# Kernel optimization log

Hardware: AMD Instinct MI355X
Metric: run time of the kernel (lower is better)

## Reference

```python
import jax, jax.numpy as jnp
import numpy as np

DIM = 768
N_HEADS = 12
HEAD_DIM = DIM // N_HEADS
SCALE = HEAD_DIM ** (-0.5)


def setup_inputs() -> dict:
    key = jax.random.key(0)
    k1, k2, k3 = jax.random.split(key, 3)
    B, S = 8, 1024
    x = jax.random.normal(k1, (B, S, DIM), dtype=jnp.float32)
    qkv_w = jax.random.normal(k2, (3 * DIM, DIM), dtype=jnp.float32) * (DIM ** -0.5)
    qkv_b = jnp.zeros((3 * DIM,), dtype=jnp.float32)
    proj_w = jax.random.normal(k3, (DIM, DIM), dtype=jnp.float32) * (DIM ** -0.5)
    proj_b = jnp.zeros((DIM,), dtype=jnp.float32)
    return {"x": x, "qkv_w": qkv_w, "qkv_b": qkv_b, "proj_w": proj_w, "proj_b": proj_b}


def reference(x, qkv_w, qkv_b, proj_w, proj_b):
    B, S, D = x.shape
    # qkv projection: (B,S,3D)
    qkv = jnp.einsum('bsd,ed->bse', x, qkv_w) + qkv_b
    qkv = qkv.reshape(B, S, 3, N_HEADS, HEAD_DIM)
    q, k, v = qkv[:, :, 0], qkv[:, :, 1], qkv[:, :, 2]  # each (B,S,H,Dh)
    # scaled dot-product attention, materializing (B,H,S,S) as the original does
    scores = jnp.einsum('bqhd,bkhd->bhqk', q, k) * SCALE
    attn = jax.nn.softmax(scores, axis=-1)
    out = jnp.einsum('bhqk,bkhd->bqhd', attn, v).reshape(B, S, D)
    # output projection
    return jnp.einsum('bsd,ed->bse', out, proj_w) + proj_b
```

## Files before the change

### kernel.cpp

```cpp
#include <hip/hip_runtime.h>
#include <hip/hip_bf16.h>


typedef __attribute__((ext_vector_type(4))) float  f32x4;
typedef __attribute__((ext_vector_type(8))) short  short8;
typedef __attribute__((ext_vector_type(4))) short  short4v;

__device__ __forceinline__ unsigned short f2bf_hw(float f) {
  return __builtin_bit_cast(unsigned short, __float2bfloat16(f));
}

#define MFMA16(a, b, c) __builtin_amdgcn_mfma_f32_16x16x32_bf16((a), (b), (c), 0, 0, 0)

#define QSCALE 0.18033688011112042f

__device__ __forceinline__ void gload_lds16(const unsigned short* g, char* lds) {
  __builtin_amdgcn_global_load_lds(
      (const __attribute__((address_space(1))) unsigned int*)g,
      (__attribute__((address_space(3))) unsigned int*)lds, 16, 0, 0);
}

__global__ __launch_bounds__(256)
void cvt3(const float* __restrict__ a, unsigned short* __restrict__ da, int na,
          const float* __restrict__ b, unsigned short* __restrict__ db, int nb,
          const float* __restrict__ c, unsigned short* __restrict__ dc)
{
  int i = blockIdx.x * 256 + threadIdx.x;
  const float* s; unsigned short* d;
  if (i < na)           { s = a; d = da; }
  else if (i < na + nb) { s = b; d = db; i -= na; }
  else                  { s = c; d = dc; i -= na + nb; }
  f32x4 v = ((const f32x4*)s)[i];
  short4v h;
  h[0] = (short)f2bf_hw(v[0]); h[1] = (short)f2bf_hw(v[1]);
  h[2] = (short)f2bf_hw(v[2]); h[3] = (short)f2bf_hw(v[3]);
  ((short4v*)d)[i] = h;
}

template<int EPI>
__global__ __launch_bounds__(256)
void gemm_bt(const unsigned short* __restrict__ A, const unsigned short* __restrict__ Wb,
             const float* __restrict__ bias,
             unsigned short* __restrict__ Qt, unsigned short* __restrict__ Kt,
             unsigned short* __restrict__ Vt, float* __restrict__ Out)
{
  __shared__ char lds[65536];
  const int tid = threadIdx.x;
  const int w = tid >> 6, l = tid & 63, lr = l & 15, lg = l >> 4;
  const int wr = w >> 1, wc = w & 1;
  const int m0 = blockIdx.x * 128, n0 = blockIdx.y * 128;
  f32x4 acc[4][4] = {};

  const int srow = tid >> 3;
  const int cb   = ((tid & 7) << 4) ^ ((srow & 7) << 4);
  const unsigned short* pA = A  + (size_t)(m0 + srow) * 768 + (cb >> 1);
  const unsigned short* pW = Wb + (size_t)(n0 + srow) * 768 + (cb >> 1);
  char* const ldsA = lds + tid * 16;
  char* const ldsW = lds + 16384 + tid * 16;

  #pragma unroll
  for (int c = 0; c < 4; ++c) gload_lds16(pA + c * 32 * 768, ldsA + c * 4096);
  #pragma unroll
  for (int c = 0; c < 4; ++c) gload_lds16(pW + c * 32 * 768, ldsW + c * 4096);
  pA += 64; pW += 64;

  for (int kt = 0; kt < 12; ++kt) {
    if (kt < 11) {
      const int nb = ((kt + 1) & 1) * 32768;
      #pragma unroll
      for (int c = 0; c < 4; ++c) gload_lds16(pA + c * 32 * 768, ldsA + nb + c * 4096);
      #pragma unroll
      for (int c = 0; c < 4; ++c) gload_lds16(pW + c * 32 * 768, ldsW + nb + c * 4096);
      pA += 64; pW += 64;
      asm volatile("s_waitcnt vmcnt(8)" ::: "memory");
    } else {
      asm volatile("s_waitcnt vmcnt(0)" ::: "memory");
    }
    __builtin_amdgcn_s_barrier();
    __builtin_amdgcn_sched_barrier(0);

    const char* Ab = lds + (kt & 1) * 32768;
    const char* Bb = Ab + 16384;
    #pragma unroll
    for (int kc = 0; kc < 2; ++kc) {
      short8 af[4], bfr[4];
      #pragma unroll
      for (int mf = 0; mf < 4; ++mf) {
        const int row = wr * 64 + mf * 16 + lr;
        af[mf] = *(const short8*)(Ab + row * 128 +
                                  ((kc * 64 + lg * 16) ^ ((row & 7) << 4)));
      }
      #pragma unroll
      for (int nf = 0; nf < 4; ++nf) {
        const int row = wc * 64 + nf * 16 + lr;
        bfr[nf] = *(const short8*)(Bb + row * 128 +
                                   ((kc * 64 + lg * 16) ^ ((row & 7) << 4)));
      }
      #pragma unroll
      for (int mf = 0; mf < 4; ++mf)
        #pragma unroll
        for (int nf = 0; nf < 4; ++nf)
          acc[mf][nf] = MFMA16(af[mf], bfr[nf], acc[mf][nf]);
    }
    __builtin_amdgcn_s_barrier();
  }

  if constexpr (EPI == 0) {
    const int tt = blockIdx.y / 6;
    const int h = (blockIdx.y % 6) * 2 + wc;
    #pragma unroll
    for (int nf = 0; nf < 4; ++nf) {
      const int dh = nf * 16 + lr;
      const float bv = bias[n0 + wc * 64 + dh];
      #pragma unroll
      for (int mf = 0; mf < 4; ++mf) {
        const int mb = m0 + wr * 64 + mf * 16 + lg * 4;
        const int b_ = mb >> 10, s_ = mb & 1023;
        f32x4 c = acc[mf][nf];
        if (tt == 0) {
          unsigned short* p = Qt + ((b_ * 12 + h) * 1024 + s_) * 64 + dh;
          #pragma unroll
          for (int j = 0; j < 4; ++j) p[j * 64] = f2bf_hw((c[j] + bv) * QSCALE);
        } else if (tt == 1) {
          unsigned short* p = Kt + ((b_ * 12 + h) * 1024 + s_) * 64 + dh;
          #pragma unroll
          for (int j = 0; j < 4; ++j) p[j * 64] = f2bf_hw(c[j] + bv);
        } else {
          short4v pk;
          #pragma unroll
          for (int j = 0; j < 4; ++j) pk[j] = (short)f2bf_hw(c[j] + bv);
          *(short4v*)(Vt + ((b_ * 12 + h) * 64 + dh) * 1024 + s_) = pk;
        }
      }
    }
  } else {
    #pragma unroll
    for (int nf = 0; nf < 4; ++nf) {
      const int e = n0 + wc * 64 + nf * 16 + lr;
      const float bv = bias[e];
      #pragma unroll
      for (int mf = 0; mf < 4; ++mf) {
        const int mb = m0 + wr * 64 + mf * 16 + lg * 4;
        #pragma unroll
        for (int j = 0; j < 4; ++j)
          Out[(size_t)(mb + j) * 768 + e] = acc[mf][nf][j] + bv;
      }
    }
  }
}

__global__ __launch_bounds__(256, 2)
void attn_fwd(const unsigned short* __restrict__ Qt,
              const unsigned short* __restrict__ Kt,
              const unsigned short* __restrict__ Vt,
              unsigned short* __restrict__ AO)
{
  __shared__ char lds[81920];
  char* Ks = lds;
  char* Vs = lds + 32768;
  char* Ps = lds + 65536;

  const int bid = blockIdx.x;
  const int bh = bid % 96, qt = bid / 96;
  const int tid = threadIdx.x, w = tid >> 6, l = tid & 63, lr = l & 15, lg = l >> 4;
  const int q0 = qt * 64 + w * 16;
  const unsigned short* Qh = Qt + bh * 65536;
  const unsigned short* Kh = Kt + bh * 65536;
  const unsigned short* Vh = Vt + bh * 65536;

  const int krow0 = tid >> 3, kcb0 = (tid & 7) << 4;
  const int vrow0 = tid >> 4, vcb0 = (tid & 15) << 4;

  const short8 aq0 = *(const short8*)(Qh + (q0 + lr) * 64 + lg * 8);
  const short8 aq1 = *(const short8*)(Qh + (q0 + lr) * 64 + 32 + lg * 8);

  #pragma unroll
  for (int c = 0; c < 4; ++c) {
    const int row = krow0 + c * 32;
    const int cb = kcb0 ^ ((row & 7) << 4);
    gload_lds16(Kh + (size_t)row * 64 + (cb >> 1), Ks + tid * 16 + c * 4096);
  }
  #pragma unroll
  for (int c = 0; c < 4; ++c) {
    const int row = vrow0 + c * 16;
    const int cb = vcb0 ^ ((row & 7) << 4);
    gload_lds16(Vh + (size_t)row * 1024 + (cb >> 1), Vs + tid * 16 + c * 4096);
  }
  __syncthreads();

  float mr = -1e30f, lsum = 0.f;
  f32x4 o[4] = {};
  char* Pw = Ps + w * 4096;

  for (int t = 0; t < 8; ++t) {
    const int cur = t & 1;
    if (t < 7) {
      const int ktn = (t + 1) * 128;
      #pragma unroll
      for (int c = 0; c < 4; ++c) {
        const int row = krow0 + c * 32;
        const int cb = kcb0 ^ ((row & 7) << 4);
        gload_lds16(Kh + (size_t)(ktn + row) * 64 + (cb >> 1),
                    Ks + (cur ^ 1) * 16384 + tid * 16 + c * 4096);
      }
      #pragma unroll
      for (int c = 0; c < 4; ++c) {
        const int row = vrow0 + c * 16;
        const int cb = vcb0 ^ ((row & 7) << 4);
        gload_lds16(Vh + (size_t)row * 1024 + ktn + (cb >> 1),
                    Vs + (cur ^ 1) * 16384 + tid * 16 + c * 4096);
      }
    }

    const char* Kb = Ks + cur * 16384;
    f32x4 sf[8];
    __builtin_amdgcn_s_setprio(1);
    #pragma unroll
    for (int kf = 0; kf < 8; ++kf) {
      const int row = kf * 16 + lr;
      const char* base = Kb + row * 128;
      const int swz = (row & 7) << 4;
      short8 b0 = *(const short8*)(base + ((lg * 16) ^ swz));
      short8 b1 = *(const short8*)(base + ((64 + lg * 16) ^ swz));
      f32x4 c = {};
      c = MFMA16(b0, aq0, c);
      c = MFMA16(b1, aq1, c);
      sf[kf] = c;
    }
    __builtin_amdgcn_s_setprio(0);

    float tm = sf[0][0];
    #pragma unroll
    for (int kf = 0; kf < 8; ++kf)
      #pragma unroll
      for (int j = 0; j < 4; ++j) tm = fmaxf(tm, sf[kf][j]);
    tm = fmaxf(tm, __shfl_xor(tm, 16));
    tm = fmaxf(tm, __shfl_xor(tm, 32));

    const float mn = fmaxf(mr, tm);
    const float corr = exp2f(mr - mn);
    float ts = 0.f;
    const int pswz = (lr & 7) << 4;
    #pragma unroll
    for (int kf = 0; kf < 8; ++kf) {
      short4v pk;
      #pragma unroll
      for (int j = 0; j < 4; ++j) {
        float p = exp2f(sf[kf][j] - mn);
        ts += p;
        pk[j] = (short)f2bf_hw(p);
      }
      *(short4v*)(Pw + lr * 256 + ((kf * 32 + lg * 8) ^ pswz)) = pk;
    }
    ts += __shfl_xor(ts, 16);
    ts += __shfl_xor(ts, 32);
    lsum = lsum * corr + ts;
    mr = mn;

    float cj[4];
    #pragma unroll
    for (int j = 0; j < 4; ++j) cj[j] = __shfl(corr, lg * 4 + j);
    #pragma unroll
    for (int cf = 0; cf < 4; ++cf)
      #pragma unroll
      for (int j = 0; j < 4; ++j) o[cf][j] *= cj[j];

    asm volatile("s_waitcnt lgkmcnt(0)" ::: "memory");
    __builtin_amdgcn_sched_barrier(0);

    const char* Vb = Vs + cur * 16384;
    __builtin_amdgcn_s_setprio(1);
    #pragma unroll
    for (int kc = 0; kc < 4; ++kc) {
      short8 pa = *(const short8*)(Pw + lr * 256 + ((kc * 64 + lg * 16) ^ pswz));
      #pragma unroll
      for (int cf = 0; cf < 4; ++cf) {
        const int row = cf * 16 + lr;
        short8 bv = *(const short8*)(Vb + row * 256 +
                                     ((kc * 64 + lg * 16) ^ ((row & 7) << 4)));
        o[cf] = MFMA16(pa, bv, o[cf]);
      }
    }
    __builtin_amdgcn_s_setprio(0);

    __syncthreads();
  }

  const float inv = 1.f / lsum;
  float ij[4];
  #pragma unroll
  for (int j = 0; j < 4; ++j) ij[j] = __shfl(inv, lg * 4 + j);
  const int b_ = bh / 12, h = bh % 12;
  #pragma unroll
  for (int cf = 0; cf < 4; ++cf)
    #pragma unroll
    for (int j = 0; j < 4; ++j)
      AO[(b_ * 1024 + q0 + lg * 4 + j) * 768 + h * 64 + cf * 16 + lr] = f2bf_hw(o[cf][j] * ij[j]);
}

extern "C" void kernel_launch(void* const* d_in, const int* in_sizes, int n_in,
                              void* d_out, int out_size, void* d_ws, size_t ws_size,
                              hipStream_t stream)
{
  const float* x      = (const float*)d_in[0];
  const float* qkv_w  = (const float*)d_in[1];
  const float* qkv_b  = (const float*)d_in[2];
  const float* proj_w = (const float*)d_in[3];
  const float* proj_b = (const float*)d_in[4];
  float* out = (float*)d_out;

  unsigned short* ws = (unsigned short*)d_ws;
  unsigned short* xb  = ws;
  unsigned short* Qt  = ws + 6291456;
  unsigned short* Kt  = Qt + 6291456;
  unsigned short* Vt  = Kt + 6291456;
  unsigned short* qwb = Vt + 6291456;
  unsigned short* pwb = qwb + 1769472;
  unsigned short* AO  = xb;

  cvt3<<<8448, 256, 0, stream>>>(x, xb, 1572864, qkv_w, qwb, 442368, proj_w, pwb);
  gemm_bt<0><<<dim3(64, 18), 256, 0, stream>>>(xb, qwb, qkv_b, Qt, Kt, Vt, nullptr);
  attn_fwd<<<1536, 256, 0, stream>>>(Qt, Kt, Vt, AO);
  gemm_bt<1><<<dim3(64, 6), 256, 0, stream>>>(AO, pwb, proj_b, nullptr, nullptr, nullptr, out);
}
```

Measured before the change: 126.6 us.

## Restructure attention: smaller KV tiles, two query sub-tiles per block, lazy rescale

The attention kernel now streams K/V in 64-key tiles instead of 128, which halves LDS use and raises the occupancy hint from 2 to 4 blocks per CU. Each block handles two 64-row query sub-tiles in sequence, and the K/V pipeline wraps around so the first tile of the second pass is prefetched. The grid is halved to match. Online-softmax rescaling is skipped unless the running max grows by more than 8 (in log2 units), the PV MFMA operands are swapped so output writes are packed per row, and the P tile is packed as bf16 pairs. The cost is twice as many loop iterations and barriers per key length, plus fewer blocks to spread across CUs.

```diff
diff --git a/kernel.cpp b/kernel.cpp
--- a/kernel.cpp
+++ b/kernel.cpp
@@ -5,9 +5,13 @@
 typedef __attribute__((ext_vector_type(4))) float  f32x4;
 typedef __attribute__((ext_vector_type(8))) short  short8;
 typedef __attribute__((ext_vector_type(4))) short  short4v;
+typedef __attribute__((ext_vector_type(2))) unsigned int uint2v;
 
 __device__ __forceinline__ unsigned short f2bf_hw(float f) {
   return __builtin_bit_cast(unsigned short, __float2bfloat16(f));
+}
+__device__ __forceinline__ unsigned int pk2bf(float a, float b) {
+  return (unsigned int)f2bf_hw(a) | ((unsigned int)f2bf_hw(b) << 16);
 }
 
 #define MFMA16(a, b, c) __builtin_amdgcn_mfma_f32_16x16x32_bf16((a), (b), (c), 0, 0, 0)
@@ -149,153 +153,141 @@
   }
 }
 
-__global__ __launch_bounds__(256, 2)
+__global__ __launch_bounds__(256, 4)
 void attn_fwd(const unsigned short* __restrict__ Qt,
               const unsigned short* __restrict__ Kt,
               const unsigned short* __restrict__ Vt,
               unsigned short* __restrict__ AO)
 {
-  __shared__ char lds[81920];
+  __shared__ char lds[40960];
   char* Ks = lds;
-  char* Vs = lds + 32768;
-  char* Ps = lds + 65536;
+  char* Vs = lds + 16384;
+  char* Ps = lds + 32768;
 
   const int bid = blockIdx.x;
   const int bh = bid % 96, qt = bid / 96;
   const int tid = threadIdx.x, w = tid >> 6, l = tid & 63, lr = l & 15, lg = l >> 4;
-  const int q0 = qt * 64 + w * 16;
   const unsigned short* Qh = Qt + bh * 65536;
   const unsigned short* Kh = Kt + bh * 65536;
   const unsigned short* Vh = Vt + bh * 65536;
-
-  const int krow0 = tid >> 3, kcb0 = (tid & 7) << 4;
-  const int vrow0 = tid >> 4, vcb0 = (tid & 15) << 4;
-
-  const short8 aq0 = *(const short8*)(Qh + (q0 + lr) * 64 + lg * 8);
-  const short8 aq1 = *(const short8*)(Qh + (q0 + lr) * 64 + 32 + lg * 8);
+  const int b_ = bh / 12, h = bh % 12;
+
+  const int srow = tid >> 3;
+  const int cb   = ((tid & 7) << 4) ^ ((srow & 7) << 4);
+  char* const ldsK = Ks + tid * 16;
+  char* const ldsV = Vs + tid * 16;
+  char* const Pw = Ps + w * 2048;
+  const int pswz = (lr & 7) << 4;
 
   #pragma unroll
-  for (int c = 0; c < 4; ++c) {
-    const int row = krow0 + c * 32;
-    const int cb = kcb0 ^ ((row & 7) << 4);
-    gload_lds16(Kh + (size_t)row * 64 + (cb >> 1), Ks + tid * 16 + c * 4096);
+  for (int c = 0; c < 2; ++c)
+    gload_lds16(Kh + (size_t)(srow + c * 32) * 64 + (cb >> 1), ldsK + c * 4096);
+  #pragma unroll
+  for (int c = 0; c < 2; ++c)
+    gload_lds16(Vh + (size_t)(srow + c * 32) * 1024 + (cb >> 1), ldsV + c * 4096);
+  __syncthreads();
+
+  for (int qs = 0; qs < 2; ++qs) {
+    const int q0 = qt * 128 + qs * 64 + w * 16;
+    const short8 aq0 = *(const short8*)(Qh + (q0 + lr) * 64 + lg * 8);
+    const short8 aq1 = *(const short8*)(Qh + (q0 + lr) * 64 + 32 + lg * 8);
+
+    float mr = -1e30f, lsum = 0.f;
+    f32x4 o[4] = {};
+
+    for (int t = 0; t < 16; ++t) {
+      const int cur = t & 1;
+      if (!(qs == 1 && t == 15)) {
+        const int nk = ((t + 1) & 15) * 64;
+        const int nb = (cur ^ 1) * 8192;
+        #pragma unroll
+        for (int c = 0; c < 2; ++c)
+          gload_lds16(Kh + (size_t)(nk + srow + c * 32) * 64 + (cb >> 1),
+                      ldsK + nb + c * 4096);
+        #pragma unroll
+        for (int c = 0; c < 2; ++c)
+          gload_lds16(Vh + (size_t)(srow + c * 32) * 1024 + nk + (cb >> 1),
+                      ldsV + nb + c * 4096);
+      }
+
+      const char* Kb = Ks + cur * 8192;
+      f32x4 sf[4];
+      __builtin_amdgcn_s_setprio(1);
+      #pragma unroll
+      for (int kf = 0; kf < 4; ++kf) {
+        const char* base = Kb + (kf * 16 + lr) * 128;
+        short8 b0 = *(const short8*)(base + ((lg * 16) ^ pswz));
+        short8 b1 = *(const short8*)(base + ((64 + lg * 16) ^ pswz));
+        f32x4 c = {};
+        c = MFMA16(b0, aq0, c);
+        c = MFMA16(b1, aq1, c);
+        sf[kf] = c;
+      }
+      __builtin_amdgcn_s_setprio(0);
+
+      float tm = fmaxf(fmaxf(sf[0][0], sf[0][1]), fmaxf(sf[0][2], sf[0][3]));
+      #pragma unroll
+      for (int kf = 1; kf < 4; ++kf)
+        tm = fmaxf(tm, fmaxf(fmaxf(sf[kf][0], sf[kf][1]), fmaxf(sf[kf][2], sf[kf][3])));
+      tm = fmaxf(tm, __shfl_xor(tm, 16));
+      tm = fmaxf(tm, __shfl_xor(tm, 32));
+
+      if (__any(tm > mr + 8.0f)) {
+        const float mn = fmaxf(mr, tm);
+        const float corr = exp2f(mr - mn);
+        lsum *= corr;
+        #pragma unroll
+        for (int cf = 0; cf < 4; ++cf)
+          #pragma unroll
+          for (int j = 0; j < 4; ++j) o[cf][j] *= corr;
+        mr = mn;
+      }
+
+      float ts = 0.f;
+      #pragma unroll
+      for (int kf = 0; kf < 4; ++kf) {
+        const float p0 = exp2f(sf[kf][0] - mr);
+        const float p1 = exp2f(sf[kf][1] - mr);
+        const float p2 = exp2f(sf[kf][2] - mr);
+        const float p3 = exp2f(sf[kf][3] - mr);
+        ts += (p0 + p1) + (p2 + p3);
+        uint2v pv; pv[0] = pk2bf(p0, p1); pv[1] = pk2bf(p2, p3);
+        *(uint2v*)(Pw + lr * 128 + ((kf * 32 + lg * 8) ^ pswz)) = pv;
+      }
+      ts += __shfl_xor(ts, 16);
+      ts += __shfl_xor(ts, 32);
+      lsum += ts;
+
+      asm volatile("s_waitcnt lgkmcnt(0)" ::: "memory");
+      __builtin_amdgcn_sched_barrier(0);
+
+      const char* Vb = Vs + cur * 8192;
+      __builtin_amdgcn_s_setprio(1);
+      #pragma unroll
+      for (int kc = 0; kc < 2; ++kc) {
+        short8 pa = *(const short8*)(Pw + lr * 128 + ((kc * 64 + lg * 16) ^ pswz));
+        #pragma unroll
+        for (int cf = 0; cf < 4; ++cf) {
+          short8 bv = *(const short8*)(Vb + (cf * 16 + lr) * 128 +
+                                       ((kc * 64 + lg * 16) ^ pswz));
+          o[cf] = MFMA16(bv, pa, o[cf]);
+        }
+      }
+      __builtin_amdgcn_s_setprio(0);
+
+      __syncthreads();
+    }
+
+    const float inv = 1.f / lsum;
+    unsigned short* aop = AO + ((size_t)(b_ * 1024 + q0 + lr)) * 768 + h * 64 + lg * 4;
+    #pragma unroll
+    for (int cf = 0; cf < 4; ++cf) {
+      uint2v pv;
+      pv[0] = pk2bf(o[cf][0] * inv, o[cf][1] * inv);
+      pv[1] = pk2bf(o[cf][2] * inv, o[cf][3] * inv);
+      *(uint2v*)(aop + cf * 16) = pv;
+    }
   }
-  #pragma unroll
-  for (int c = 0; c < 4; ++c) {
-    const int row = vrow0 + c * 16;
-    const int cb = vcb0 ^ ((row & 7) << 4);
-    gload_lds16(Vh + (size_t)row * 1024 + (cb >> 1), Vs + tid * 16 + c * 4096);
-  }
-  __syncthreads();
-
-  float mr = -1e30f, lsum = 0.f;
-  f32x4 o[4] = {};
-  char* Pw = Ps + w * 4096;
-
-  for (int t = 0; t < 8; ++t) {
-    const int cur = t & 1;
-    if (t < 7) {
-      const int ktn = (t + 1) * 128;
-      #pragma unroll
-      for (int c = 0; c < 4; ++c) {
-        const int row = krow0 + c * 32;
-        const int cb = kcb0 ^ ((row & 7) << 4);
-        gload_lds16(Kh + (size_t)(ktn + row) * 64 + (cb >> 1),
-                    Ks + (cur ^ 1) * 16384 + tid * 16 + c * 4096);
-      }
-      #pragma unroll
-      for (int c = 0; c < 4; ++c) {
-        const int row = vrow0 + c * 16;
-        const int cb = vcb0 ^ ((row & 7) << 4);
-        gload_lds16(Vh + (size_t)row * 1024 + ktn + (cb >> 1),
-                    Vs + (cur ^ 1) * 16384 + tid * 16 + c * 4096);
-      }
-    }
-
-    const char* Kb = Ks + cur * 16384;
-    f32x4 sf[8];
-    __builtin_amdgcn_s_setprio(1);
-    #pragma unroll
-    for (int kf = 0; kf < 8; ++kf) {
-      const int row = kf * 16 + lr;
-      const char* base = Kb + row * 128;
-      const int swz = (row & 7) << 4;
-      short8 b0 = *(const short8*)(base + ((lg * 16) ^ swz));
-      short8 b1 = *(const short8*)(base + ((64 + lg * 16) ^ swz));
-      f32x4 c = {};
-      c = MFMA16(b0, aq0, c);
-      c = MFMA16(b1, aq1, c);
-      sf[kf] = c;
-    }
-    __builtin_amdgcn_s_setprio(0);
-
-    float tm = sf[0][0];
-    #pragma unroll
-    for (int kf = 0; kf < 8; ++kf)
-      #pragma unroll
-      for (int j = 0; j < 4; ++j) tm = fmaxf(tm, sf[kf][j]);
-    tm = fmaxf(tm, __shfl_xor(tm, 16));
-    tm = fmaxf(tm, __shfl_xor(tm, 32));
-
-    const float mn = fmaxf(mr, tm);
-    const float corr = exp2f(mr - mn);
-    float ts = 0.f;
-    const int pswz = (lr & 7) << 4;
-    #pragma unroll
-    for (int kf = 0; kf < 8; ++kf) {
-      short4v pk;
-      #pragma unroll
-      for (int j = 0; j < 4; ++j) {
-        float p = exp2f(sf[kf][j] - mn);
-        ts += p;
-        pk[j] = (short)f2bf_hw(p);
-      }
-      *(short4v*)(Pw + lr * 256 + ((kf * 32 + lg * 8) ^ pswz)) = pk;
-    }
-    ts += __shfl_xor(ts, 16);
-    ts += __shfl_xor(ts, 32);
-    lsum = lsum * corr + ts;
-    mr = mn;
-
-    float cj[4];
-    #pragma unroll
-    for (int j = 0; j < 4; ++j) cj[j] = __shfl(corr, lg * 4 + j);
-    #pragma unroll
-    for (int cf = 0; cf < 4; ++cf)
-      #pragma unroll
-      for (int j = 0; j < 4; ++j) o[cf][j] *= cj[j];
-
-    asm volatile("s_waitcnt lgkmcnt(0)" ::: "memory");
-    __builtin_amdgcn_sched_barrier(0);
-
-    const char* Vb = Vs + cur * 16384;
-    __builtin_amdgcn_s_setprio(1);
-    #pragma unroll
-    for (int kc = 0; kc < 4; ++kc) {
-      short8 pa = *(const short8*)(Pw + lr * 256 + ((kc * 64 + lg * 16) ^ pswz));
-      #pragma unroll
-      for (int cf = 0; cf < 4; ++cf) {
-        const int row = cf * 16 + lr;
-        short8 bv = *(const short8*)(Vb + row * 256 +
-                                     ((kc * 64 + lg * 16) ^ ((row & 7) << 4)));
-        o[cf] = MFMA16(pa, bv, o[cf]);
-      }
-    }
-    __builtin_amdgcn_s_setprio(0);
-
-    __syncthreads();
-  }
-
-  const float inv = 1.f / lsum;
-  float ij[4];
-  #pragma unroll
-  for (int j = 0; j < 4; ++j) ij[j] = __shfl(inv, lg * 4 + j);
-  const int b_ = bh / 12, h = bh % 12;
-  #pragma unroll
-  for (int cf = 0; cf < 4; ++cf)
-    #pragma unroll
-    for (int j = 0; j < 4; ++j)
-      AO[(b_ * 1024 + q0 + lg * 4 + j) * 768 + h * 64 + cf * 16 + lr] = f2bf_hw(o[cf][j] * ij[j]);
 }
 
 extern "C" void kernel_launch(void* const* d_in, const int* in_sizes, int n_in,
@@ -320,6 +312,6 @@
 
   cvt3<<<8448, 256, 0, stream>>>(x, xb, 1572864, qkv_w, qwb, 442368, proj_w, pwb);
   gemm_bt<0><<<dim3(64, 18), 256, 0, stream>>>(xb, qwb, qkv_b, Qt, Kt, Vt, nullptr);
-  attn_fwd<<<1536, 256, 0, stream>>>(Qt, Kt, Vt, AO);
+  attn_fwd<<<768, 256, 0, stream>>>(Qt, Kt, Vt, AO);
   gemm_bt<1><<<dim3(64, 6), 256, 0, stream>>>(AO, pwb, proj_b, nullptr, nullptr, nullptr, out);
 }
```

Measured after the change: 125.4 us. About the same (-1.0%).
